# Optimization experiments

Hardware: AMD Instinct MI355X
Metric: run time of the kernel (lower is better)

Reference implementation:

```python
import jax, jax.numpy as jnp
import numpy as np

THRESHOLD = 0.005


def _build_laplacian(x, threshold=THRESHOLD):
    # x: [B, C, F]; cosine-correlation adjacency over channels, built with no grad.
    norm = jnp.sqrt(jnp.sum(x * x, axis=2, keepdims=True))          # [B, C, 1]
    denom = jnp.einsum('bcx,bdx->bcd', norm, norm)                  # [B, C, C]
    num = jnp.einsum('bcf,bdf->bcd', x, x)                          # [B, C, C]
    corr = num / denom
    A = jnp.where(jax.nn.relu(corr) > threshold, 1.0, 0.0)          # binarized adjacency
    deg = jnp.sum(A, axis=2)                                        # [B, C]; >=1 (self-corr==1)
    d_inv_sqrt = 1.0 / jnp.sqrt(deg)
    # D^{-1/2} A D^{-1/2} as elementwise row/col scaling (diag inverse is reciprocal)
    L = A * d_inv_sqrt[:, :, None] * d_inv_sqrt[:, None, :]
    return jax.lax.stop_gradient(L)


def setup_inputs() -> dict:
    key = jax.random.key(0)
    k = jax.random.split(key, 5)
    F = 512
    stdv = 1.0 / np.sqrt(F)
    x = jax.random.normal(k[0], (8, 2048, F), dtype=jnp.float32)
    W1 = jax.random.uniform(k[1], (1, F, F), dtype=jnp.float32, minval=-stdv, maxval=stdv)
    b1 = jax.random.uniform(k[2], (1,), dtype=jnp.float32, minval=-stdv, maxval=stdv)
    W2 = jax.random.uniform(k[3], (1, F, F), dtype=jnp.float32, minval=-stdv, maxval=stdv)
    b2 = jax.random.uniform(k[4], (1,), dtype=jnp.float32, minval=-stdv, maxval=stdv)
    return {"x": x, "W1": W1, "b1": b1, "W2": W2, "b2": b2}


def reference(x, W1, b1, W2, b2):
    L = _build_laplacian(x)                                         # [B, C, C]
    h = x                                                           # [B, C, F]
    for W, b in ((W1, b1), (W2, b2)):
        lx = jnp.einsum('bcd,bdf->bcf', L, h)                       # graph propagation
        h = jax.nn.relu(jnp.einsum('bcf,fg->bcg', lx, W[0]) + b)    # linear + scalar bias + relu
    return h
```

## Files before the change

kernel.cpp:

```cpp
#include <hip/hip_runtime.h>
#include <hip/hip_bf16.h>
#include <cstdint>
#include <cstddef>

#define B_ 8
#define C_ 2048
#define F_ 512
#define TTILES 32
#define NPAIRS 528
#define BAND 0.015f
#define FLAGCAP (1u << 18)

typedef short bf16x8 __attribute__((ext_vector_type(8)));
typedef float f32x4 __attribute__((ext_vector_type(4)));


__device__ __forceinline__ ushort bf16hi(float v) {
  return __builtin_bit_cast(unsigned short, __float2bfloat16(v));
}

__device__ __forceinline__ int swz2048(int flat) {
  return (flat & 7) * 256 + (flat >> 3);
}

__global__ __launch_bounds__(64) void kzero1(uint32_t* __restrict__ flagn) {
  if (threadIdx.x == 0) *flagn = 0u;
}

__global__ __launch_bounds__(256) void ksplit(const float* __restrict__ x,
                                              ushort* __restrict__ xhi,
                                              ushort* __restrict__ xlo) {
  size_t i = ((size_t)blockIdx.x * 256 + threadIdx.x) * 8;
  float4 v0 = *reinterpret_cast<const float4*>(x + i);
  float4 v1 = *reinterpret_cast<const float4*>(x + i + 4);
  float vv[8] = {v0.x, v0.y, v0.z, v0.w, v1.x, v1.y, v1.z, v1.w};
  ushort h[8], lo[8];
#pragma unroll
  for (int j = 0; j < 8; ++j) {
    ushort hh = bf16hi(vv[j]);
    float hf = __bfloat162float(__builtin_bit_cast(__hip_bfloat16, hh));
    h[j] = hh; lo[j] = bf16hi(vv[j] - hf);
  }
  *reinterpret_cast<uint4*>(xhi + i) = *reinterpret_cast<uint4*>(h);
  *reinterpret_cast<uint4*>(xlo + i) = *reinterpret_cast<uint4*>(lo);
}

__global__ __launch_bounds__(256) void kwsplit(const float* __restrict__ W1,
                                               const float* __restrict__ W2,
                                               ushort* __restrict__ wtbuf) {
  const float* W = blockIdx.z ? W2 : W1;
  ushort* whi = wtbuf + (size_t)blockIdx.z * 524288;
  ushort* wlo = whi + 262144;
  int k0 = blockIdx.x * 64, n0 = blockIdx.y * 64, tid = threadIdx.x;
  __shared__ float t[64][65];
#pragma unroll
// ... 15 lines not shown
      float v = t[g * 8 + j][n];
      ushort hh = bf16hi(v);
      float hf = __bfloat162float(__builtin_bit_cast(__hip_bfloat16, hh));
      h8[j] = hh; l8[j] = bf16hi(v - hf);
    }
    size_t ga = (size_t)(n0 + n) * 512 + k0 + g * 8;
    *reinterpret_cast<uint4*>(&whi[ga]) = *reinterpret_cast<uint4*>(h8);
    *reinterpret_cast<uint4*>(&wlo[ga]) = *reinterpret_cast<uint4*>(l8);
  }
}

__global__ __launch_bounds__(256) void knorm(const float* __restrict__ x,
                                             double* __restrict__ nrm) {
  int row = blockIdx.x * 4 + (threadIdx.x >> 6);
  int lane = threadIdx.x & 63;
  const float4* xr = reinterpret_cast<const float4*>(x + (size_t)row * F_);
  float4 v1 = xr[lane];
  float4 v2 = xr[lane + 64];
  double s = (double)v1.x * v1.x + (double)v1.y * v1.y +
             (double)v1.z * v1.z + (double)v1.w * v1.w +
             (double)v2.x * v2.x + (double)v2.y * v2.y +
             (double)v2.z * v2.z + (double)v2.w * v2.w;
#pragma unroll
  for (int off = 32; off > 0; off >>= 1) s += __shfl_down(s, off, 64);
  if (lane == 0) nrm[row] = sqrt(s);
}

__global__ __launch_bounds__(256) void kgram2(const ushort* __restrict__ xhi,
                                              const ushort* __restrict__ xlo,
                                              const double* __restrict__ nrm,
                                              uint32_t* __restrict__ bits,
                                              uint32_t* __restrict__ flagn,
                                              uint32_t* __restrict__ flags) {
  int b = blockIdx.y;
  int tt = (int)blockIdx.x, I = 0;
  while (tt >= TTILES - I) { tt -= TTILES - I; ++I; }
  int J = I + tt;
  bool offdiag = (I != J);
  int c0 = I * 64, d0 = J * 64;
  int tid = threadIdx.x;
  int l = tid & 63, w = tid >> 6;
  int wc = w >> 1, wf = w & 1;
  int lg = l >> 4, li = l & 15;

  __shared__ ushort sm[4 * 64 * 64];
  __shared__ uint32_t lb[64][2];
  __shared__ uint32_t lbT[64][2];

  f32x4 acc[2][2];
#pragma unroll
  for (int m = 0; m < 2; ++m)
#pragma unroll
    for (int n = 0; n < 2; ++n) acc[m][n] = (f32x4){0.f, 0.f, 0.f, 0.f};

  const size_t xbase = (size_t)b * C_ * F_;

  for (int kc = 0; kc < F_ / 64; ++kc) {
    __syncthreads();
#pragma unroll
    for (int s = 0; s < 8; ++s) {
      int is = w + s * 4;
      int tile = is >> 3, sub = is & 7;
      const ushort* src = (tile & 1) ? xlo : xhi;
      int rbase = (tile < 2) ? c0 : d0;
      int row = sub * 8 + (l >> 3);
      int g = l & 7;
      uint4 v = *reinterpret_cast<const uint4*>(
          src + xbase + (size_t)(rbase + row) * F_ + kc * 64 + g * 8);
      int ldsoff = tile * 4096 + row * 64 + ((g ^ (row & 7)) * 8);
      *reinterpret_cast<uint4*>(&sm[ldsoff]) = v;
    }
    __syncthreads();
#pragma unroll
    for (int kk = 0; kk < 2; ++kk) {
      bf16x8 ah[2], al[2], bh[2], bl[2];
#pragma unroll
      for (int m = 0; m < 2; ++m) {
        int row = wc * 32 + m * 16 + li;
        int off = row * 64 + (((kk * 4 + lg) ^ (row & 7)) * 8);
        ah[m] = *reinterpret_cast<const bf16x8*>(&sm[off]);
        al[m] = *reinterpret_cast<const bf16x8*>(&sm[4096 + off]);
      }
#pragma unroll
      for (int n = 0; n < 2; ++n) {
        int row = wf * 32 + n * 16 + li;
        int off = row * 64 + (((kk * 4 + lg) ^ (row & 7)) * 8);
        bh[n] = *reinterpret_cast<const bf16x8*>(&sm[8192 + off]);
        bl[n] = *reinterpret_cast<const bf16x8*>(&sm[12288 + off]);
      }
#pragma unroll
      for (int m = 0; m < 2; ++m)
#pragma unroll
        for (int n = 0; n < 2; ++n) {
          acc[m][n] = __builtin_amdgcn_mfma_f32_16x16x32_bf16(ah[m], bh[n], acc[m][n], 0, 0, 0);
          acc[m][n] = __builtin_amdgcn_mfma_f32_16x16x32_bf16(ah[m], bl[n], acc[m][n], 0, 0, 0);
          acc[m][n] = __builtin_amdgcn_mfma_f32_16x16x32_bf16(al[m], bh[n], acc[m][n], 0, 0, 0);
        }
    }
  }

  double ncv[2][4], ndv[2];
#pragma unroll
  for (int m = 0; m < 2; ++m)
#pragma unroll
    for (int q = 0; q < 4; ++q)
      ncv[m][q] = nrm[b * C_ + c0 + wc * 32 + m * 16 + lg * 4 + q];
#pragma unroll
  for (int n = 0; n < 2; ++n)
    ndv[n] = nrm[b * C_ + d0 + wf * 32 + n * 16 + li];

#pragma unroll
  for (int m = 0; m < 2; ++m) {
#pragma unroll
    for (int q = 0; q < 4; ++q) {
      uint32_t wv = 0;
#pragma unroll
      for (int n = 0; n < 2; ++n) {
        float num = acc[m][n][q];
        float tq = (float)(0.005 * ncv[m][q] * ndv[n]);
        bool bit = num > tq;
        if (fabsf(num - tq) < BAND) {
          uint32_t idx = atomicAdd(flagn, 1u);
          if (idx < FLAGCAP) {
            int cc = c0 + wc * 32 + m * 16 + lg * 4 + q;
            int dd = d0 + wf * 32 + n * 16 + li;
            flags[idx] = ((uint32_t)b << 22) | ((uint32_t)cc << 11) | (uint32_t)dd;
          }
        }
        unsigned long long bal = __ballot(bit);
        uint32_t b16 = (uint32_t)((bal >> (lg * 16)) & 0xFFFFull);
        wv |= b16 << (n * 16);
// ... 43 lines not shown
#pragma unroll
    for (int off = 32; off > 0; off >>= 1) s += __shfl_down(s, off, 64);
    if (l == 0) {
      bool bit = s > 0.005 * nrm[b * C_ + c] * nrm[b * C_ + d];
      uint32_t* wcd = bits + (((size_t)b * C_ + c) << 6) + (d >> 5);
      uint32_t* wdc = bits + (((size_t)b * C_ + d) << 6) + (c >> 5);
      uint32_t mcd = 1u << (d & 31), mdc = 1u << (c & 31);
      if (bit) { atomicOr(wcd, mcd);  atomicOr(wdc, mdc); }
      else     { atomicAnd(wcd, ~mcd); atomicAnd(wdc, ~mdc); }
    }
  }
}

__global__ __launch_bounds__(256) void kdeg(const uint32_t* __restrict__ bits,
                                            float* __restrict__ sinv) {
  int row = blockIdx.x * 256 + threadIdx.x;
  const uint4* p = reinterpret_cast<const uint4*>(bits + ((size_t)row << 6));
  uint32_t s = 0;
#pragma unroll
  for (int i = 0; i < 16; ++i) {
    uint4 v = p[i];
    s += __popc(v.x) + __popc(v.y) + __popc(v.z) + __popc(v.w);
  }
  sinv[row] = 1.0f / sqrtf((float)s);
}

__global__ __launch_bounds__(256) void kgemm_mfma(const ushort* __restrict__ ahi,
                                                  const ushort* __restrict__ alo,
                                                  const ushort* __restrict__ wthi,
                                                  const ushort* __restrict__ wtlo,
                                                  const float* __restrict__ sinv,
                                                  ushort* __restrict__ gthi,
                                                  ushort* __restrict__ gtlo) {
  int flat = (int)blockIdx.y * 256 + (int)blockIdx.x;
  int nid = swz2048(flat);
  int m0 = (nid & 255) * 64, n0 = (nid >> 8) * 64;
  int tid = threadIdx.x;
  int l = tid & 63, w = tid >> 6;
  int wc = w >> 1, wf = w & 1;
  int lg = l >> 4, li = l & 15;

  __shared__ ushort smA[2 * 4096];
  __shared__ ushort smW[2 * 4096];

  f32x4 acc[2][2];
#pragma unroll
  for (int m = 0; m < 2; ++m)
#pragma unroll
    for (int n = 0; n < 2; ++n) acc[m][n] = (f32x4){0.f, 0.f, 0.f, 0.f};

  for (int kc = 0; kc < 8; ++kc) {
    int k0 = kc * 64;
    __syncthreads();
#pragma unroll
    for (int it = 0; it < 2; ++it) {
      int slot = tid + it * 256;
      int row = slot >> 3, grp = slot & 7;
      int loff = row * 64 + ((grp ^ (row & 7)) * 8);
      size_t ga = (size_t)(m0 + row) * 512 + k0 + grp * 8;
      *reinterpret_cast<uint4*>(&smA[loff])        = *reinterpret_cast<const uint4*>(ahi + ga);
      *reinterpret_cast<uint4*>(&smA[4096 + loff]) = *reinterpret_cast<const uint4*>(alo + ga);
      size_t gw = (size_t)(n0 + row) * 512 + k0 + grp * 8;
      *reinterpret_cast<uint4*>(&smW[loff])        = *reinterpret_cast<const uint4*>(wthi + gw);
      *reinterpret_cast<uint4*>(&smW[4096 + loff]) = *reinterpret_cast<const uint4*>(wtlo + gw);
    }
    __syncthreads();
#pragma unroll
    for (int kk = 0; kk < 2; ++kk) {
      bf16x8 ah[2], al[2], wh[2], wl[2];
#pragma unroll
      for (int m = 0; m < 2; ++m) {
        int row = wc * 32 + m * 16 + li;
        int off = row * 64 + (((kk * 4 + lg) ^ (row & 7)) * 8);
        ah[m] = *reinterpret_cast<const bf16x8*>(&smA[off]);
        al[m] = *reinterpret_cast<const bf16x8*>(&smA[4096 + off]);
      }
#pragma unroll
      for (int n = 0; n < 2; ++n) {
        int row = wf * 32 + n * 16 + li;
        int off = row * 64 + (((kk * 4 + lg) ^ (row & 7)) * 8);
        wh[n] = *reinterpret_cast<const bf16x8*>(&smW[off]);
        wl[n] = *reinterpret_cast<const bf16x8*>(&smW[4096 + off]);
      }
#pragma unroll
      for (int m = 0; m < 2; ++m)
#pragma unroll
        for (int n = 0; n < 2; ++n) {
          acc[m][n] = __builtin_amdgcn_mfma_f32_16x16x32_bf16(ah[m], wh[n], acc[m][n], 0, 0, 0);
          acc[m][n] = __builtin_amdgcn_mfma_f32_16x16x32_bf16(ah[m], wl[n], acc[m][n], 0, 0, 0);
          acc[m][n] = __builtin_amdgcn_mfma_f32_16x16x32_bf16(al[m], wh[n], acc[m][n], 0, 0, 0);
          acc[m][n] = __builtin_amdgcn_mfma_f32_16x16x32_bf16(al[m], wl[n], acc[m][n], 0, 0, 0);
        }
    }
  }

  int b = m0 >> 11, cb = m0 & 2047;
#pragma unroll
  for (int m = 0; m < 2; ++m) {
    int rowl = wc * 32 + m * 16 + lg * 4;
    f32x4 sc = *reinterpret_cast<const f32x4*>(&sinv[m0 + rowl]);
#pragma unroll
    for (int n = 0; n < 2; ++n) {
      int f = n0 + wf * 32 + n * 16 + li;
      ushort h4[4], l4[4];
#pragma unroll
      for (int q = 0; q < 4; ++q) {
        float v = sc[q] * acc[m][n][q];
        ushort hh = bf16hi(v);
        float hf = __bfloat162float(__builtin_bit_cast(__hip_bfloat16, hh));
        h4[q] = hh; l4[q] = bf16hi(v - hf);
      }
      size_t ga = ((size_t)b * F_ + f) * C_ + cb + rowl;
      *reinterpret_cast<ushort4*>(&gthi[ga]) = *reinterpret_cast<ushort4*>(h4);
      *reinterpret_cast<ushort4*>(&gtlo[ga]) = *reinterpret_cast<ushort4*>(l4);
    }
  }
}

__global__ __launch_bounds__(256) void kprop_mfma(const ushort* __restrict__ gthi,
                                                  const ushort* __restrict__ gtlo,
                                                  const float* __restrict__ sinv,
                                                  const uint32_t* __restrict__ bits,
                                                  const float* __restrict__ bias,
                                                  ushort* __restrict__ ohi,
                                                  ushort* __restrict__ olo,
                                                  float* __restrict__ of32) {
  int nid = swz2048((int)blockIdx.x);
  int c0 = (nid & 31) * 64, f0 = ((nid >> 5) & 7) * 64, b = nid >> 8;
  int tid = threadIdx.x;
  int l = tid & 63, w = tid >> 6;
  int wc = w >> 1, wf = w & 1;
  int lg = l >> 4, li = l & 15;

  __shared__ ushort smv[2 * 4096];
  __shared__ uint32_t blds[64][68];

  const uint32_t* bp = bits + (((size_t)b * C_ + c0) << 6);
#pragma unroll
  for (int t = 0; t < 4; ++t) {
    int gi = (t * 256 + tid) * 4;
    uint4 q = *reinterpret_cast<const uint4*>(bp + gi);
    int row = gi >> 6, col = gi & 63;
    *reinterpret_cast<uint4*>(&blds[row][col]) = q;
  }

  f32x4 acc[2][2];
#pragma unroll
  for (int m = 0; m < 2; ++m)
#pragma unroll
    for (int n = 0; n < 2; ++n) acc[m][n] = (f32x4){0.f, 0.f, 0.f, 0.f};

  const float* sv = sinv + b * C_;

  for (int d0 = 0; d0 < C_; d0 += 64) {
    __syncthreads();
#pragma unroll
    for (int it = 0; it < 2; ++it) {
      int slot = tid + it * 256;
      int row = slot >> 3, grp = slot & 7;
      int loff = row * 64 + ((grp ^ (row & 7)) * 8);
      size_t ga = ((size_t)b * F_ + f0 + row) * C_ + d0 + grp * 8;
      *reinterpret_cast<uint4*>(&smv[loff])        = *reinterpret_cast<const uint4*>(gthi + ga);
      *reinterpret_cast<uint4*>(&smv[4096 + loff]) = *reinterpret_cast<const uint4*>(gtlo + ga);
    }
    __syncthreads();

    int wbase = d0 >> 5;
#pragma unroll
    for (int kk = 0; kk < 2; ++kk) {
      uint32_t wd0 = blds[wc * 32 + li][wbase + kk];
      uint32_t wd1 = blds[wc * 32 + 16 + li][wbase + kk];
      uint32_t by0 = (wd0 >> (lg * 8)) & 0xFFu;
      uint32_t by1 = (wd1 >> (lg * 8)) & 0xFFu;
      bf16x8 a0, a1;
#pragma unroll
      for (int j = 0; j < 8; ++j) {
        a0[j] = (short)(((by0 >> j) & 1u) ? 0x3F80 : 0);
        a1[j] = (short)(((by1 >> j) & 1u) ? 0x3F80 : 0);
      }
      bf16x8 bh0, bl0, bh1, bl1;
      {
        int row = wf * 32 + li;
        int off = row * 64 + (((kk * 4 + lg) ^ (row & 7)) * 8);
        bh0 = *reinterpret_cast<const bf16x8*>(&smv[off]);
        bl0 = *reinterpret_cast<const bf16x8*>(&smv[4096 + off]);
      }
      {
        int row = wf * 32 + 16 + li;
        int off = row * 64 + (((kk * 4 + lg) ^ (row & 7)) * 8);
        bh1 = *reinterpret_cast<const bf16x8*>(&smv[off]);
        bl1 = *reinterpret_cast<const bf16x8*>(&smv[4096 + off]);
      }
      acc[0][0] = __builtin_amdgcn_mfma_f32_16x16x32_bf16(a0, bh0, acc[0][0], 0, 0, 0);
      acc[0][0] = __builtin_amdgcn_mfma_f32_16x16x32_bf16(a0, bl0, acc[0][0], 0, 0, 0);
      acc[0][1] = __builtin_amdgcn_mfma_f32_16x16x32_bf16(a0, bh1, acc[0][1], 0, 0, 0);
      acc[0][1] = __builtin_amdgcn_mfma_f32_16x16x32_bf16(a0, bl1, acc[0][1], 0, 0, 0);
      acc[1][0] = __builtin_amdgcn_mfma_f32_16x16x32_bf16(a1, bh0, acc[1][0], 0, 0, 0);
      acc[1][0] = __builtin_amdgcn_mfma_f32_16x16x32_bf16(a1, bl0, acc[1][0], 0, 0, 0);
      acc[1][1] = __builtin_amdgcn_mfma_f32_16x16x32_bf16(a1, bh1, acc[1][1], 0, 0, 0);
      acc[1][1] = __builtin_amdgcn_mfma_f32_16x16x32_bf16(a1, bl1, acc[1][1], 0, 0, 0);
    }
  }

  float bb = bias[0];
#pragma unroll
  for (int m = 0; m < 2; ++m) {
    int rowb = c0 + wc * 32 + m * 16 + lg * 4;
    f32x4 sc = *reinterpret_cast<const f32x4*>(&sv[rowb]);
#pragma unroll
    for (int n = 0; n < 2; ++n) {
      int col = f0 + wf * 32 + n * 16 + li;
      if (of32) {
#pragma unroll
        for (int q = 0; q < 4; ++q) {
          float o = fmaxf(sc[q] * acc[m][n][q] + bb, 0.f);
          of32[((size_t)b * C_ + rowb + q) * F_ + col] = o;
        }
      } else {
#pragma unroll
        for (int q = 0; q < 4; ++q) {
          float o = fmaxf(sc[q] * acc[m][n][q] + bb, 0.f);
          ushort hh = bf16hi(o);
          float hf = __bfloat162float(__builtin_bit_cast(__hip_bfloat16, hh));
          size_t ga = ((size_t)b * C_ + rowb + q) * F_ + col;
          ohi[ga] = hh;
          olo[ga] = bf16hi(o - hf);
        }
      }
    }
  }
}

extern "C" void kernel_launch(void* const* d_in, const int* in_sizes, int n_in,
                              void* d_out, int out_size, void* d_ws, size_t ws_size,
                              hipStream_t stream) {
  (void)in_sizes; (void)n_in; (void)out_size; (void)ws_size;
  const float* x  = (const float*)d_in[0];
  const float* W1 = (const float*)d_in[1];
  const float* b1 = (const float*)d_in[2];
  const float* W2 = (const float*)d_in[3];
  const float* b2 = (const float*)d_in[4];
  float* out = (float*)d_out;

  char* ws = (char*)d_ws;
  double*   nrm   = (double*)(ws);
  uint32_t* bits  = (uint32_t*)(ws + 131072);
  float*    sinv  = (float*)(ws + 4325376);
  uint32_t* flagn = (uint32_t*)(ws + 4390912);
  uint32_t* flags = (uint32_t*)(ws + 4391168);
  ushort*   wt    = (ushort*)(ws + 5439744);
  ushort*   xhi   = (ushort*)(ws + 7536896);
  ushort*   xlo   = (ushort*)(ws + 24314112);
  ushort*   gthi  = (ushort*)(ws + 41091328);
  ushort*   gtlo  = (ushort*)(ws + 57868544);
  ushort*   wt1hi = wt, *wt1lo = wt + 262144, *wt2hi = wt + 524288, *wt2lo = wt + 786432;

  kzero1<<<dim3(1), 64, 0, stream>>>(flagn);
  ksplit<<<dim3(B_ * C_ * F_ / 2048), 256, 0, stream>>>(x, xhi, xlo);
  knorm<<<dim3(B_ * C_ / 4), 256, 0, stream>>>(x, nrm);
  kwsplit<<<dim3(8, 8, 2), 256, 0, stream>>>(W1, W2, wt);
  kgram2<<<dim3(NPAIRS, B_), 256, 0, stream>>>(xhi, xlo, nrm, bits, flagn, flags);
  krepair<<<dim3(256), 256, 0, stream>>>(x, nrm, flagn, flags, bits);
  kdeg<<<dim3(B_ * C_ / 256), 256, 0, stream>>>(bits, sinv);

  kgemm_mfma<<<dim3(256, 8), 256, 0, stream>>>(xhi, xlo, wt1hi, wt1lo, sinv, gthi, gtlo);
  kprop_mfma<<<dim3(2048), 256, 0, stream>>>(gthi, gtlo, sinv, bits, b1, xhi, xlo, nullptr);
  kgemm_mfma<<<dim3(256, 8), 256, 0, stream>>>(xhi, xlo, wt2hi, wt2lo, sinv, gthi, gtlo);
  kprop_mfma<<<dim3(2048), 256, 0, stream>>>(gthi, gtlo, sinv, bits, b2, nullptr, nullptr, out);
}
```

Before: 514.8 us.

## Register-prefetch next K chunk in gram, gemm, and prop kernels; retile prop to 128 rows

The Gram, GEMM and propagation kernels now load the next K chunk from global memory into registers while the current chunk is computed from LDS. This replaces the two-syncthreads load-then-compute pattern with explicit barriers and lgkmcnt waits. The block-to-tile mapping is changed so the batch index is innermost, aiming at XCD/L2 locality. The GEMM epilogue transposes through LDS to make global stores coalesced, and the prop kernel uses 128-row tiles with 4 N-subtiles per wave to reuse each loaded G tile more. The cost is more registers and larger LDS use, which may lower occupancy.

```diff
diff --git a/kernel.cpp b/kernel.cpp
--- a/kernel.cpp
+++ b/kernel.cpp
@@ -17,10 +17,6 @@
 
 __device__ __forceinline__ ushort bf16hi(float v) {
   return __builtin_bit_cast(unsigned short, __float2bfloat16(v));
-}
-
-__device__ __forceinline__ int swz2048(int flat) {
-  return (flat & 7) * 256 + (flat >> 3);
 }
 
 __global__ __launch_bounds__(64) void kzero1(uint32_t* __restrict__ flagn) {
@@ -102,8 +98,9 @@
                                               uint32_t* __restrict__ bits,
                                               uint32_t* __restrict__ flagn,
                                               uint32_t* __restrict__ flags) {
-  int b = blockIdx.y;
-  int tt = (int)blockIdx.x, I = 0;
+  int flat = (int)blockIdx.x;
+  int b = flat & 7;
+  int tt = flat >> 3, I = 0;
   while (tt >= TTILES - I) { tt -= TTILES - I; ++I; }
   int J = I + tt;
   bool offdiag = (I != J);
@@ -125,22 +122,37 @@
 
   const size_t xbase = (size_t)b * C_ * F_;
 
-  for (int kc = 0; kc < F_ / 64; ++kc) {
-    __syncthreads();
-#pragma unroll
-    for (int s = 0; s < 8; ++s) {
-      int is = w + s * 4;
-      int tile = is >> 3, sub = is & 7;
-      const ushort* src = (tile & 1) ? xlo : xhi;
-      int rbase = (tile < 2) ? c0 : d0;
-      int row = sub * 8 + (l >> 3);
-      int g = l & 7;
-      uint4 v = *reinterpret_cast<const uint4*>(
-          src + xbase + (size_t)(rbase + row) * F_ + kc * 64 + g * 8);
-      int ldsoff = tile * 4096 + row * 64 + ((g ^ (row & 7)) * 8);
-      *reinterpret_cast<uint4*>(&sm[ldsoff]) = v;
-    }
-    __syncthreads();
+  const ushort* gs[8]; int lo8[8];
+#pragma unroll
+  for (int s = 0; s < 8; ++s) {
+    int is = w + s * 4;
+    int tile = is >> 3, sub = is & 7;
+    const ushort* src = (tile & 1) ? xlo : xhi;
+    int rbase = (tile < 2) ? c0 : d0;
+    int row = sub * 8 + (l >> 3);
+    int g = l & 7;
+    gs[s] = src + xbase + (size_t)(rbase + row) * F_ + g * 8;
+    lo8[s] = tile * 4096 + row * 64 + ((g ^ (row & 7)) * 8);
+  }
+
+  uint4 rX[2][8];
+#pragma unroll
+  for (int s = 0; s < 8; ++s) rX[0][s] = *reinterpret_cast<const uint4*>(gs[s]);
+
+#pragma unroll
+  for (int kc = 0; kc < 8; ++kc) {
+    int cur = kc & 1;
+    __builtin_amdgcn_sched_barrier(0);
+    __builtin_amdgcn_s_barrier();
+#pragma unroll
+    for (int s = 0; s < 8; ++s)
+      *reinterpret_cast<uint4*>(&sm[lo8[s]]) = rX[cur][s];
+#pragma unroll
+    for (int s = 0; s < 8; ++s)
+      rX[cur ^ 1][s] = *reinterpret_cast<const uint4*>(gs[s] + ((kc + 1) & 7) * 64);
+    asm volatile("s_waitcnt lgkmcnt(0)" ::: "memory");
+    __builtin_amdgcn_sched_barrier(0);
+    __builtin_amdgcn_s_barrier();
 #pragma unroll
     for (int kk = 0; kk < 2; ++kk) {
       bf16x8 ah[2], al[2], bh[2], bl[2];
@@ -276,16 +288,29 @@
                                                   const float* __restrict__ sinv,
                                                   ushort* __restrict__ gthi,
                                                   ushort* __restrict__ gtlo) {
-  int flat = (int)blockIdx.y * 256 + (int)blockIdx.x;
-  int nid = swz2048(flat);
-  int m0 = (nid & 255) * 64, n0 = (nid >> 8) * 64;
+  int flat = (int)blockIdx.x;
+  int b = flat & 7, rest = flat >> 3;
+  int mtl = rest & 31, nt = rest >> 5;
+  int m0 = b * C_ + mtl * 64;
+  int n0 = nt * 64;
   int tid = threadIdx.x;
   int l = tid & 63, w = tid >> 6;
   int wc = w >> 1, wf = w & 1;
   int lg = l >> 4, li = l & 15;
 
-  __shared__ ushort smA[2 * 4096];
-  __shared__ ushort smW[2 * 4096];
+  __shared__ ushort smem[16384];
+
+  int ldso[2];
+  const ushort* gA[2][2]; const ushort* gW[2][2];
+#pragma unroll
+  for (int it = 0; it < 2; ++it) {
+    int slot = tid + it * 256, row = slot >> 3, grp = slot & 7;
+    ldso[it] = row * 64 + ((grp ^ (row & 7)) * 8);
+    size_t ga = (size_t)(m0 + row) * 512 + grp * 8;
+    gA[it][0] = ahi + ga; gA[it][1] = alo + ga;
+    size_t gw = (size_t)(n0 + row) * 512 + grp * 8;
+    gW[it][0] = wthi + gw; gW[it][1] = wtlo + gw;
+  }
 
   f32x4 acc[2][2];
 #pragma unroll
@@ -293,22 +318,38 @@
 #pragma unroll
     for (int n = 0; n < 2; ++n) acc[m][n] = (f32x4){0.f, 0.f, 0.f, 0.f};
 
+  uint4 rA[2][2][2];
+#pragma unroll
+  for (int it = 0; it < 2; ++it) {
+    rA[0][it][0] = *reinterpret_cast<const uint4*>(gA[it][0]);
+    rA[0][it][1] = *reinterpret_cast<const uint4*>(gA[it][1]);
+  }
+
+#pragma unroll
   for (int kc = 0; kc < 8; ++kc) {
+    int cur = kc & 1;
     int k0 = kc * 64;
-    __syncthreads();
+    __builtin_amdgcn_sched_barrier(0);
+    __builtin_amdgcn_s_barrier();
 #pragma unroll
     for (int it = 0; it < 2; ++it) {
-      int slot = tid + it * 256;
-      int row = slot >> 3, grp = slot & 7;
-      int loff = row * 64 + ((grp ^ (row & 7)) * 8);
-      size_t ga = (size_t)(m0 + row) * 512 + k0 + grp * 8;
-      *reinterpret_cast<uint4*>(&smA[loff])        = *reinterpret_cast<const uint4*>(ahi + ga);
-      *reinterpret_cast<uint4*>(&smA[4096 + loff]) = *reinterpret_cast<const uint4*>(alo + ga);
-      size_t gw = (size_t)(n0 + row) * 512 + k0 + grp * 8;
-      *reinterpret_cast<uint4*>(&smW[loff])        = *reinterpret_cast<const uint4*>(wthi + gw);
-      *reinterpret_cast<uint4*>(&smW[4096 + loff]) = *reinterpret_cast<const uint4*>(wtlo + gw);
-    }
-    __syncthreads();
+      *reinterpret_cast<uint4*>(&smem[ldso[it]])        = rA[cur][it][0];
+      *reinterpret_cast<uint4*>(&smem[4096 + ldso[it]]) = rA[cur][it][1];
+    }
+#pragma unroll
+    for (int it = 0; it < 2; ++it) {
+      int nk = ((kc + 1) & 7) * 64;
+      rA[cur ^ 1][it][0] = *reinterpret_cast<const uint4*>(gA[it][0] + nk);
+      rA[cur ^ 1][it][1] = *reinterpret_cast<const uint4*>(gA[it][1] + nk);
+    }
+#pragma unroll
+    for (int it = 0; it < 2; ++it) {
+      *reinterpret_cast<uint4*>(&smem[8192 + ldso[it]])  = *reinterpret_cast<const uint4*>(gW[it][0] + k0);
+      *reinterpret_cast<uint4*>(&smem[12288 + ldso[it]]) = *reinterpret_cast<const uint4*>(gW[it][1] + k0);
+    }
+    asm volatile("s_waitcnt lgkmcnt(0)" ::: "memory");
+    __builtin_amdgcn_sched_barrier(0);
+    __builtin_amdgcn_s_barrier();
 #pragma unroll
     for (int kk = 0; kk < 2; ++kk) {
       bf16x8 ah[2], al[2], wh[2], wl[2];
@@ -316,15 +357,15 @@
       for (int m = 0; m < 2; ++m) {
         int row = wc * 32 + m * 16 + li;
         int off = row * 64 + (((kk * 4 + lg) ^ (row & 7)) * 8);
-        ah[m] = *reinterpret_cast<const bf16x8*>(&smA[off]);
-        al[m] = *reinterpret_cast<const bf16x8*>(&smA[4096 + off]);
+        ah[m] = *reinterpret_cast<const bf16x8*>(&smem[off]);
+        al[m] = *reinterpret_cast<const bf16x8*>(&smem[4096 + off]);
       }
 #pragma unroll
       for (int n = 0; n < 2; ++n) {
         int row = wf * 32 + n * 16 + li;
         int off = row * 64 + (((kk * 4 + lg) ^ (row & 7)) * 8);
-        wh[n] = *reinterpret_cast<const bf16x8*>(&smW[off]);
-        wl[n] = *reinterpret_cast<const bf16x8*>(&smW[4096 + off]);
+        wh[n] = *reinterpret_cast<const bf16x8*>(&smem[8192 + off]);
+        wl[n] = *reinterpret_cast<const bf16x8*>(&smem[12288 + off]);
       }
 #pragma unroll
       for (int m = 0; m < 2; ++m)
@@ -338,14 +379,14 @@
     }
   }
 
-  int b = m0 >> 11, cb = m0 & 2047;
+  __syncthreads();
 #pragma unroll
   for (int m = 0; m < 2; ++m) {
-    int rowl = wc * 32 + m * 16 + lg * 4;
-    f32x4 sc = *reinterpret_cast<const f32x4*>(&sinv[m0 + rowl]);
+    int dl = wc * 32 + m * 16 + lg * 4;
+    f32x4 sc = *reinterpret_cast<const f32x4*>(&sinv[m0 + dl]);
 #pragma unroll
     for (int n = 0; n < 2; ++n) {
-      int f = n0 + wf * 32 + n * 16 + li;
+      int fl = wf * 32 + n * 16 + li;
       ushort h4[4], l4[4];
 #pragma unroll
       for (int q = 0; q < 4; ++q) {
@@ -354,12 +395,70 @@
         float hf = __bfloat162float(__builtin_bit_cast(__hip_bfloat16, hh));
         h4[q] = hh; l4[q] = bf16hi(v - hf);
       }
-      size_t ga = ((size_t)b * F_ + f) * C_ + cb + rowl;
-      *reinterpret_cast<ushort4*>(&gthi[ga]) = *reinterpret_cast<ushort4*>(h4);
-      *reinterpret_cast<ushort4*>(&gtlo[ga]) = *reinterpret_cast<ushort4*>(l4);
-    }
-  }
-}
+      *reinterpret_cast<ushort4*>(&smem[fl * 68 + dl])        = *reinterpret_cast<ushort4*>(h4);
+      *reinterpret_cast<ushort4*>(&smem[4352 + fl * 68 + dl]) = *reinterpret_cast<ushort4*>(l4);
+    }
+  }
+  __syncthreads();
+  {
+    int fl = tid >> 2, seg = tid & 3;
+    int cb = mtl * 64;
+    int lo = fl * 68 + seg * 16;
+    size_t ga = ((size_t)b * F_ + n0 + fl) * C_ + cb + seg * 16;
+    uint4 p0 = *reinterpret_cast<const uint4*>(&smem[lo]);
+    uint4 p1 = *reinterpret_cast<const uint4*>(&smem[lo + 8]);
+    *reinterpret_cast<uint4*>(&gthi[ga])     = p0;
+    *reinterpret_cast<uint4*>(&gthi[ga + 8]) = p1;
+    uint4 q0 = *reinterpret_cast<const uint4*>(&smem[4352 + lo]);
+    uint4 q1 = *reinterpret_cast<const uint4*>(&smem[4352 + lo + 8]);
+    *reinterpret_cast<uint4*>(&gtlo[ga])     = q0;
+    *reinterpret_cast<uint4*>(&gtlo[ga + 8]) = q1;
+  }
+}
+
+#define PROP_CHUNK(D, USE, PF, DN)                                            \
+  {                                                                           \
+    __builtin_amdgcn_sched_barrier(0);                                        \
+    __builtin_amdgcn_s_barrier();                                             \
+    _Pragma("unroll")                                                         \
+    for (int it = 0; it < 2; ++it) {                                          \
+      *reinterpret_cast<uint4*>(&smv[ldso[it]])        = USE[it][0];          \
+      *reinterpret_cast<uint4*>(&smv[4096 + ldso[it]]) = USE[it][1];          \
+    }                                                                         \
+    _Pragma("unroll")                                                         \
+    for (int it = 0; it < 2; ++it) {                                          \
+      PF[it][0] = *reinterpret_cast<const uint4*>(gsh[it] + (DN));            \
+      PF[it][1] = *reinterpret_cast<const uint4*>(gsl[it] + (DN));            \
+    }                                                                         \
+    asm volatile("s_waitcnt lgkmcnt(0)" ::: "memory");                        \
+    __builtin_amdgcn_sched_barrier(0);                                        \
+    __builtin_amdgcn_s_barrier();                                             \
+    int wbase = (D) >> 5;                                                     \
+    _Pragma("unroll")                                                         \
+    for (int kk = 0; kk < 2; ++kk) {                                          \
+      uint32_t wd0 = blds[w32 + li][wbase + kk];                              \
+      uint32_t wd1 = blds[w32 + 16 + li][wbase + kk];                         \
+      uint32_t by0 = (wd0 >> (lg * 8)) & 0xFFu;                               \
+      uint32_t by1 = (wd1 >> (lg * 8)) & 0xFFu;                               \
+      bf16x8 a0, a1;                                                          \
+      _Pragma("unroll")                                                       \
+      for (int j = 0; j < 8; ++j) {                                           \
+        a0[j] = (short)(((by0 >> j) & 1u) ? 0x3F80 : 0);                      \
+        a1[j] = (short)(((by1 >> j) & 1u) ? 0x3F80 : 0);                      \
+      }                                                                       \
+      _Pragma("unroll")                                                       \
+      for (int n = 0; n < 4; ++n) {                                           \
+        int row = n * 16 + li;                                                \
+        int off = row * 64 + (((kk * 4 + lg) ^ (row & 7)) * 8);               \
+        bf16x8 bh = *reinterpret_cast<const bf16x8*>(&smv[off]);              \
+        bf16x8 bl = *reinterpret_cast<const bf16x8*>(&smv[4096 + off]);       \
+        acc[0][n] = __builtin_amdgcn_mfma_f32_16x16x32_bf16(a0, bh, acc[0][n], 0, 0, 0); \
+        acc[0][n] = __builtin_amdgcn_mfma_f32_16x16x32_bf16(a0, bl, acc[0][n], 0, 0, 0); \
+        acc[1][n] = __builtin_amdgcn_mfma_f32_16x16x32_bf16(a1, bh, acc[1][n], 0, 0, 0); \
+        acc[1][n] = __builtin_amdgcn_mfma_f32_16x16x32_bf16(a1, bl, acc[1][n], 0, 0, 0); \
+      }                                                                       \
+    }                                                                         \
+  }
 
 __global__ __launch_bounds__(256) void kprop_mfma(const ushort* __restrict__ gthi,
                                                   const ushort* __restrict__ gtlo,
@@ -369,91 +468,64 @@
                                                   ushort* __restrict__ ohi,
                                                   ushort* __restrict__ olo,
                                                   float* __restrict__ of32) {
-  int nid = swz2048((int)blockIdx.x);
-  int c0 = (nid & 31) * 64, f0 = ((nid >> 5) & 7) * 64, b = nid >> 8;
+  int flat = (int)blockIdx.x;
+  int b = flat & 7, rest = flat >> 3;
+  int ct = rest & 15, ft = rest >> 4;
+  int c0 = ct * 128, f0 = ft * 64;
   int tid = threadIdx.x;
   int l = tid & 63, w = tid >> 6;
-  int wc = w >> 1, wf = w & 1;
   int lg = l >> 4, li = l & 15;
-
-  __shared__ ushort smv[2 * 4096];
-  __shared__ uint32_t blds[64][68];
+  int w32 = w * 32;
+
+  __shared__ ushort smv[8192];
+  __shared__ uint32_t blds[128][68];
 
   const uint32_t* bp = bits + (((size_t)b * C_ + c0) << 6);
 #pragma unroll
-  for (int t = 0; t < 4; ++t) {
+  for (int t = 0; t < 8; ++t) {
     int gi = (t * 256 + tid) * 4;
     uint4 q = *reinterpret_cast<const uint4*>(bp + gi);
     int row = gi >> 6, col = gi & 63;
     *reinterpret_cast<uint4*>(&blds[row][col]) = q;
   }
 
-  f32x4 acc[2][2];
+  int ldso[2];
+  const ushort* gsh[2]; const ushort* gsl[2];
+#pragma unroll
+  for (int it = 0; it < 2; ++it) {
+    int s = tid + it * 256, row = s >> 3, grp = s & 7;
+    ldso[it] = row * 64 + ((grp ^ (row & 7)) * 8);
+    size_t ga = ((size_t)b * F_ + f0 + row) * (size_t)C_ + grp * 8;
+    gsh[it] = gthi + ga; gsl[it] = gtlo + ga;
+  }
+
+  f32x4 acc[2][4];
 #pragma unroll
   for (int m = 0; m < 2; ++m)
 #pragma unroll
-    for (int n = 0; n < 2; ++n) acc[m][n] = (f32x4){0.f, 0.f, 0.f, 0.f};
+    for (int n = 0; n < 4; ++n) acc[m][n] = (f32x4){0.f, 0.f, 0.f, 0.f};
+
+  uint4 rA[2][2], rB[2][2];
+#pragma unroll
+  for (int it = 0; it < 2; ++it) {
+    rA[it][0] = *reinterpret_cast<const uint4*>(gsh[it]);
+    rA[it][1] = *reinterpret_cast<const uint4*>(gsl[it]);
+  }
+
+  for (int d0 = 0; d0 < C_; d0 += 128) {
+    PROP_CHUNK(d0,      rA, rB, d0 + 64);
+    PROP_CHUNK(d0 + 64, rB, rA, (d0 + 128) & (C_ - 1));
+  }
 
   const float* sv = sinv + b * C_;
-
-  for (int d0 = 0; d0 < C_; d0 += 64) {
-    __syncthreads();
-#pragma unroll
-    for (int it = 0; it < 2; ++it) {
-      int slot = tid + it * 256;
-      int row = slot >> 3, grp = slot & 7;
-      int loff = row * 64 + ((grp ^ (row & 7)) * 8);
-      size_t ga = ((size_t)b * F_ + f0 + row) * C_ + d0 + grp * 8;
-      *reinterpret_cast<uint4*>(&smv[loff])        = *reinterpret_cast<const uint4*>(gthi + ga);
-      *reinterpret_cast<uint4*>(&smv[4096 + loff]) = *reinterpret_cast<const uint4*>(gtlo + ga);
-    }
-    __syncthreads();
-
-    int wbase = d0 >> 5;
-#pragma unroll
-    for (int kk = 0; kk < 2; ++kk) {
-      uint32_t wd0 = blds[wc * 32 + li][wbase + kk];
-      uint32_t wd1 = blds[wc * 32 + 16 + li][wbase + kk];
-      uint32_t by0 = (wd0 >> (lg * 8)) & 0xFFu;
-      uint32_t by1 = (wd1 >> (lg * 8)) & 0xFFu;
-      bf16x8 a0, a1;
-#pragma unroll
-      for (int j = 0; j < 8; ++j) {
-        a0[j] = (short)(((by0 >> j) & 1u) ? 0x3F80 : 0);
-        a1[j] = (short)(((by1 >> j) & 1u) ? 0x3F80 : 0);
-      }
-      bf16x8 bh0, bl0, bh1, bl1;
-      {
-        int row = wf * 32 + li;
-        int off = row * 64 + (((kk * 4 + lg) ^ (row & 7)) * 8);
-        bh0 = *reinterpret_cast<const bf16x8*>(&smv[off]);
-        bl0 = *reinterpret_cast<const bf16x8*>(&smv[4096 + off]);
-      }
-      {
-        int row = wf * 32 + 16 + li;
-        int off = row * 64 + (((kk * 4 + lg) ^ (row & 7)) * 8);
-        bh1 = *reinterpret_cast<const bf16x8*>(&smv[off]);
-        bl1 = *reinterpret_cast<const bf16x8*>(&smv[4096 + off]);
-      }
-      acc[0][0] = __builtin_amdgcn_mfma_f32_16x16x32_bf16(a0, bh0, acc[0][0], 0, 0, 0);
-      acc[0][0] = __builtin_amdgcn_mfma_f32_16x16x32_bf16(a0, bl0, acc[0][0], 0, 0, 0);
-      acc[0][1] = __builtin_amdgcn_mfma_f32_16x16x32_bf16(a0, bh1, acc[0][1], 0, 0, 0);
-      acc[0][1] = __builtin_amdgcn_mfma_f32_16x16x32_bf16(a0, bl1, acc[0][1], 0, 0, 0);
-      acc[1][0] = __builtin_amdgcn_mfma_f32_16x16x32_bf16(a1, bh0, acc[1][0], 0, 0, 0);
-      acc[1][0] = __builtin_amdgcn_mfma_f32_16x16x32_bf16(a1, bl0, acc[1][0], 0, 0, 0);
-      acc[1][1] = __builtin_amdgcn_mfma_f32_16x16x32_bf16(a1, bh1, acc[1][1], 0, 0, 0);
-      acc[1][1] = __builtin_amdgcn_mfma_f32_16x16x32_bf16(a1, bl1, acc[1][1], 0, 0, 0);
-    }
-  }
-
   float bb = bias[0];
 #pragma unroll
   for (int m = 0; m < 2; ++m) {
-    int rowb = c0 + wc * 32 + m * 16 + lg * 4;
+    int rowb = c0 + w32 + m * 16 + lg * 4;
     f32x4 sc = *reinterpret_cast<const f32x4*>(&sv[rowb]);
 #pragma unroll
-    for (int n = 0; n < 2; ++n) {
-      int col = f0 + wf * 32 + n * 16 + li;
+    for (int n = 0; n < 4; ++n) {
+      int col = f0 + n * 16 + li;
       if (of32) {
 #pragma unroll
         for (int q = 0; q < 4; ++q) {
@@ -503,12 +575,12 @@
   ksplit<<<dim3(B_ * C_ * F_ / 2048), 256, 0, stream>>>(x, xhi, xlo);
   knorm<<<dim3(B_ * C_ / 4), 256, 0, stream>>>(x, nrm);
   kwsplit<<<dim3(8, 8, 2), 256, 0, stream>>>(W1, W2, wt);
-  kgram2<<<dim3(NPAIRS, B_), 256, 0, stream>>>(xhi, xlo, nrm, bits, flagn, flags);
+  kgram2<<<dim3(NPAIRS * B_), 256, 0, stream>>>(xhi, xlo, nrm, bits, flagn, flags);
   krepair<<<dim3(256), 256, 0, stream>>>(x, nrm, flagn, flags, bits);
   kdeg<<<dim3(B_ * C_ / 256), 256, 0, stream>>>(bits, sinv);
 
-  kgemm_mfma<<<dim3(256, 8), 256, 0, stream>>>(xhi, xlo, wt1hi, wt1lo, sinv, gthi, gtlo);
-  kprop_mfma<<<dim3(2048), 256, 0, stream>>>(gthi, gtlo, sinv, bits, b1, xhi, xlo, nullptr);
-  kgemm_mfma<<<dim3(256, 8), 256, 0, stream>>>(xhi, xlo, wt2hi, wt2lo, sinv, gthi, gtlo);
-  kprop_mfma<<<dim3(2048), 256, 0, stream>>>(gthi, gtlo, sinv, bits, b2, nullptr, nullptr, out);
-}
+  kgemm_mfma<<<dim3(2048), 256, 0, stream>>>(xhi, xlo, wt1hi, wt1lo, sinv, gthi, gtlo);
+  kprop_mfma<<<dim3(1024), 256, 0, stream>>>(gthi, gtlo, sinv, bits, b1, xhi, xlo, nullptr);
+  kgemm_mfma<<<dim3(2048), 256, 0, stream>>>(xhi, xlo, wt2hi, wt2lo, sinv, gthi, gtlo);
+  kprop_mfma<<<dim3(1024), 256, 0, stream>>>(gthi, gtlo, sinv, bits, b2, nullptr, nullptr, out);
+}
```

Result: slower. 785.8 us (+52.6%).

## Double-buffer LDS via direct global-to-LDS loads across gram, gemm and propagation kernels

Applied to the files above, without the earlier changes.

Replaces the register-staged global-to-LDS copies in kgram2, kgemm_mfma and kprop_mfma with global_load_lds direct loads into a double-buffered LDS ring, so the next K-chunk is fetched while the current one feeds MFMA. It also remaps block indices so the batch is the fastest-varying dimension, stages the transposed gemm output through LDS for coalesced 16-byte stores, and doubles the propagation tile to 128 rows per block. The cost is more LDS per block, which may lower occupancy, and it relies on the swizzled source addressing matching the layout the readers expect.

```diff
diff --git a/kernel.cpp b/kernel.cpp
--- a/kernel.cpp
+++ b/kernel.cpp
@@ -19,8 +19,10 @@
   return __builtin_bit_cast(unsigned short, __float2bfloat16(v));
 }
 
-__device__ __forceinline__ int swz2048(int flat) {
-  return (flat & 7) * 256 + (flat >> 3);
+__device__ __forceinline__ void gload16(const void* g, void* l) {
+  __builtin_amdgcn_global_load_lds(
+      (const __attribute__((address_space(1))) void*)g,
+      (__attribute__((address_space(3))) void*)l, 16, 0, 0);
 }
 
 __global__ __launch_bounds__(64) void kzero1(uint32_t* __restrict__ flagn) {
@@ -102,8 +104,9 @@
                                               uint32_t* __restrict__ bits,
                                               uint32_t* __restrict__ flagn,
                                               uint32_t* __restrict__ flags) {
-  int b = blockIdx.y;
-  int tt = (int)blockIdx.x, I = 0;
+  int flat = (int)blockIdx.x;
+  int b = flat & 7;
+  int tt = flat >> 3, I = 0;
   while (tt >= TTILES - I) { tt -= TTILES - I; ++I; }
   int J = I + tt;
   bool offdiag = (I != J);
@@ -112,35 +115,39 @@
   int l = tid & 63, w = tid >> 6;
   int wc = w >> 1, wf = w & 1;
   int lg = l >> 4, li = l & 15;
-
-  __shared__ ushort sm[4 * 64 * 64];
+  int rin = l >> 3, grp = l & 7;
+
+  __shared__ ushort sm[2][16384];
   __shared__ uint32_t lb[64][2];
   __shared__ uint32_t lbT[64][2];
 
+  const size_t xbase = (size_t)b * C_ * F_;
+
+  auto stage = [&](int buf, int kc) {
+#pragma unroll
+    for (int i = 0; i < 8; ++i) {
+      int c = w * 8 + i;
+      int t = c >> 3, sub = c & 7;
+      const ushort* src = (t & 1) ? xlo : xhi;
+      int rbase = (t < 2) ? c0 : d0;
+      int row = sub * 8 + rin;
+      gload16(src + xbase + (size_t)(rbase + row) * F_ + kc * 64 + ((grp ^ rin) << 3),
+              &sm[buf][t * 4096 + sub * 512]);
+    }
+  };
+
   f32x4 acc[2][2];
 #pragma unroll
   for (int m = 0; m < 2; ++m)
 #pragma unroll
     for (int n = 0; n < 2; ++n) acc[m][n] = (f32x4){0.f, 0.f, 0.f, 0.f};
 
-  const size_t xbase = (size_t)b * C_ * F_;
-
-  for (int kc = 0; kc < F_ / 64; ++kc) {
-    __syncthreads();
-#pragma unroll
-    for (int s = 0; s < 8; ++s) {
-      int is = w + s * 4;
-      int tile = is >> 3, sub = is & 7;
-      const ushort* src = (tile & 1) ? xlo : xhi;
-      int rbase = (tile < 2) ? c0 : d0;
-      int row = sub * 8 + (l >> 3);
-      int g = l & 7;
-      uint4 v = *reinterpret_cast<const uint4*>(
-          src + xbase + (size_t)(rbase + row) * F_ + kc * 64 + g * 8);
-      int ldsoff = tile * 4096 + row * 64 + ((g ^ (row & 7)) * 8);
-      *reinterpret_cast<uint4*>(&sm[ldsoff]) = v;
-    }
-    __syncthreads();
+  stage(0, 0);
+  __syncthreads();
+  for (int kc = 0; kc < 8; ++kc) {
+    int buf = kc & 1;
+    if (kc < 7) stage(buf ^ 1, kc + 1);
+    const ushort* sb = sm[buf];
 #pragma unroll
     for (int kk = 0; kk < 2; ++kk) {
       bf16x8 ah[2], al[2], bh[2], bl[2];
@@ -148,15 +155,15 @@
       for (int m = 0; m < 2; ++m) {
         int row = wc * 32 + m * 16 + li;
         int off = row * 64 + (((kk * 4 + lg) ^ (row & 7)) * 8);
-        ah[m] = *reinterpret_cast<const bf16x8*>(&sm[off]);
-        al[m] = *reinterpret_cast<const bf16x8*>(&sm[4096 + off]);
+        ah[m] = *reinterpret_cast<const bf16x8*>(&sb[off]);
+        al[m] = *reinterpret_cast<const bf16x8*>(&sb[4096 + off]);
       }
 #pragma unroll
       for (int n = 0; n < 2; ++n) {
         int row = wf * 32 + n * 16 + li;
         int off = row * 64 + (((kk * 4 + lg) ^ (row & 7)) * 8);
-        bh[n] = *reinterpret_cast<const bf16x8*>(&sm[8192 + off]);
-        bl[n] = *reinterpret_cast<const bf16x8*>(&sm[12288 + off]);
+        bh[n] = *reinterpret_cast<const bf16x8*>(&sb[8192 + off]);
+        bl[n] = *reinterpret_cast<const bf16x8*>(&sb[12288 + off]);
       }
 #pragma unroll
       for (int m = 0; m < 2; ++m)
@@ -167,6 +174,7 @@
           acc[m][n] = __builtin_amdgcn_mfma_f32_16x16x32_bf16(al[m], bh[n], acc[m][n], 0, 0, 0);
         }
     }
+    __syncthreads();
   }
 
   double ncv[2][4], ndv[2];
@@ -276,16 +284,34 @@
                                                   const float* __restrict__ sinv,
                                                   ushort* __restrict__ gthi,
                                                   ushort* __restrict__ gtlo) {
-  int flat = (int)blockIdx.y * 256 + (int)blockIdx.x;
-  int nid = swz2048(flat);
-  int m0 = (nid & 255) * 64, n0 = (nid >> 8) * 64;
+  int flat = (int)blockIdx.x;
+  int b = flat & 7, rest = flat >> 3;
+  int mtl = rest & 31, nt = rest >> 5;
+  int m0 = b * C_ + mtl * 64;
+  int n0 = nt * 64;
   int tid = threadIdx.x;
   int l = tid & 63, w = tid >> 6;
   int wc = w >> 1, wf = w & 1;
   int lg = l >> 4, li = l & 15;
-
-  __shared__ ushort smA[2 * 4096];
-  __shared__ ushort smW[2 * 4096];
+  int rin = l >> 3, grp = l & 7;
+
+  __shared__ ushort sm[2][16384];
+
+  auto stage = [&](int buf, int kc) {
+#pragma unroll
+    for (int i = 0; i < 8; ++i) {
+      int c = w * 8 + i;
+      int t = c >> 3, sub = c & 7;
+      int row = sub * 8 + rin;
+      const ushort* src; size_t rb;
+      if (t == 0)      { src = ahi;  rb = (size_t)(m0 + row) * F_; }
+      else if (t == 1) { src = alo;  rb = (size_t)(m0 + row) * F_; }
+      else if (t == 2) { src = wthi; rb = (size_t)(n0 + row) * F_; }
+      else             { src = wtlo; rb = (size_t)(n0 + row) * F_; }
+      gload16(src + rb + kc * 64 + ((grp ^ rin) << 3),
+              &sm[buf][t * 4096 + sub * 512]);
+    }
+  };
 
   f32x4 acc[2][2];
 #pragma unroll
@@ -293,22 +319,12 @@
 #pragma unroll
     for (int n = 0; n < 2; ++n) acc[m][n] = (f32x4){0.f, 0.f, 0.f, 0.f};
 
+  stage(0, 0);
+  __syncthreads();
   for (int kc = 0; kc < 8; ++kc) {
-    int k0 = kc * 64;
-    __syncthreads();
-#pragma unroll
-    for (int it = 0; it < 2; ++it) {
-      int slot = tid + it * 256;
-      int row = slot >> 3, grp = slot & 7;
-      int loff = row * 64 + ((grp ^ (row & 7)) * 8);
-      size_t ga = (size_t)(m0 + row) * 512 + k0 + grp * 8;
-      *reinterpret_cast<uint4*>(&smA[loff])        = *reinterpret_cast<const uint4*>(ahi + ga);
-      *reinterpret_cast<uint4*>(&smA[4096 + loff]) = *reinterpret_cast<const uint4*>(alo + ga);
-      size_t gw = (size_t)(n0 + row) * 512 + k0 + grp * 8;
-      *reinterpret_cast<uint4*>(&smW[loff])        = *reinterpret_cast<const uint4*>(wthi + gw);
-      *reinterpret_cast<uint4*>(&smW[4096 + loff]) = *reinterpret_cast<const uint4*>(wtlo + gw);
-    }
-    __syncthreads();
+    int buf = kc & 1;
+    if (kc < 7) stage(buf ^ 1, kc + 1);
+    const ushort* sb = sm[buf];
 #pragma unroll
     for (int kk = 0; kk < 2; ++kk) {
       bf16x8 ah[2], al[2], wh[2], wl[2];
@@ -316,15 +332,15 @@
       for (int m = 0; m < 2; ++m) {
         int row = wc * 32 + m * 16 + li;
         int off = row * 64 + (((kk * 4 + lg) ^ (row & 7)) * 8);
-        ah[m] = *reinterpret_cast<const bf16x8*>(&smA[off]);
-        al[m] = *reinterpret_cast<const bf16x8*>(&smA[4096 + off]);
+        ah[m] = *reinterpret_cast<const bf16x8*>(&sb[off]);
+        al[m] = *reinterpret_cast<const bf16x8*>(&sb[4096 + off]);
       }
 #pragma unroll
       for (int n = 0; n < 2; ++n) {
         int row = wf * 32 + n * 16 + li;
         int off = row * 64 + (((kk * 4 + lg) ^ (row & 7)) * 8);
-        wh[n] = *reinterpret_cast<const bf16x8*>(&smW[off]);
-        wl[n] = *reinterpret_cast<const bf16x8*>(&smW[4096 + off]);
+        wh[n] = *reinterpret_cast<const bf16x8*>(&sb[8192 + off]);
+        wl[n] = *reinterpret_cast<const bf16x8*>(&sb[12288 + off]);
       }
 #pragma unroll
       for (int m = 0; m < 2; ++m)
@@ -336,16 +352,17 @@
           acc[m][n] = __builtin_amdgcn_mfma_f32_16x16x32_bf16(al[m], wl[n], acc[m][n], 0, 0, 0);
         }
     }
-  }
-
-  int b = m0 >> 11, cb = m0 & 2047;
+    __syncthreads();
+  }
+
+  ushort* tb = &sm[0][0];
 #pragma unroll
   for (int m = 0; m < 2; ++m) {
-    int rowl = wc * 32 + m * 16 + lg * 4;
-    f32x4 sc = *reinterpret_cast<const f32x4*>(&sinv[m0 + rowl]);
+    int dl = wc * 32 + m * 16 + lg * 4;
+    f32x4 sc = *reinterpret_cast<const f32x4*>(&sinv[m0 + dl]);
 #pragma unroll
     for (int n = 0; n < 2; ++n) {
-      int f = n0 + wf * 32 + n * 16 + li;
+      int fl = wf * 32 + n * 16 + li;
       ushort h4[4], l4[4];
 #pragma unroll
       for (int q = 0; q < 4; ++q) {
@@ -354,10 +371,19 @@
         float hf = __bfloat162float(__builtin_bit_cast(__hip_bfloat16, hh));
         h4[q] = hh; l4[q] = bf16hi(v - hf);
       }
-      size_t ga = ((size_t)b * F_ + f) * C_ + cb + rowl;
-      *reinterpret_cast<ushort4*>(&gthi[ga]) = *reinterpret_cast<ushort4*>(h4);
-      *reinterpret_cast<ushort4*>(&gtlo[ga]) = *reinterpret_cast<ushort4*>(l4);
-    }
+      *reinterpret_cast<ushort4*>(&tb[fl * 72 + dl])        = *reinterpret_cast<ushort4*>(h4);
+      *reinterpret_cast<ushort4*>(&tb[4608 + fl * 72 + dl]) = *reinterpret_cast<ushort4*>(l4);
+    }
+  }
+  __syncthreads();
+  {
+    int fl = tid >> 2, seg = tid & 3;
+    int lo = fl * 72 + seg * 16;
+    size_t ga = ((size_t)b * F_ + n0 + fl) * C_ + mtl * 64 + seg * 16;
+    *reinterpret_cast<uint4*>(&gthi[ga])     = *reinterpret_cast<const uint4*>(&tb[lo]);
+    *reinterpret_cast<uint4*>(&gthi[ga + 8]) = *reinterpret_cast<const uint4*>(&tb[lo + 8]);
+    *reinterpret_cast<uint4*>(&gtlo[ga])     = *reinterpret_cast<const uint4*>(&tb[4608 + lo]);
+    *reinterpret_cast<uint4*>(&gtlo[ga + 8]) = *reinterpret_cast<const uint4*>(&tb[4608 + lo + 8]);
   }
 }
 
@@ -369,51 +395,57 @@
                                                   ushort* __restrict__ ohi,
                                                   ushort* __restrict__ olo,
                                                   float* __restrict__ of32) {
-  int nid = swz2048((int)blockIdx.x);
-  int c0 = (nid & 31) * 64, f0 = ((nid >> 5) & 7) * 64, b = nid >> 8;
+  int flat = (int)blockIdx.x;
+  int b = flat & 7, rest = flat >> 3;
+  int ct = rest & 15, ft = rest >> 4;
+  int c0 = ct * 128, f0 = ft * 64;
   int tid = threadIdx.x;
   int l = tid & 63, w = tid >> 6;
-  int wc = w >> 1, wf = w & 1;
   int lg = l >> 4, li = l & 15;
-
-  __shared__ ushort smv[2 * 4096];
-  __shared__ uint32_t blds[64][68];
+  int rin = l >> 3, grp = l & 7;
+  int w32 = w * 32;
+
+  __shared__ ushort smv[2][8192];
+  __shared__ uint32_t blds[128][68];
 
   const uint32_t* bp = bits + (((size_t)b * C_ + c0) << 6);
 #pragma unroll
-  for (int t = 0; t < 4; ++t) {
+  for (int t = 0; t < 8; ++t) {
     int gi = (t * 256 + tid) * 4;
     uint4 q = *reinterpret_cast<const uint4*>(bp + gi);
     int row = gi >> 6, col = gi & 63;
     *reinterpret_cast<uint4*>(&blds[row][col]) = q;
   }
 
-  f32x4 acc[2][2];
+  auto stage = [&](int buf, int dd) {
+#pragma unroll
+    for (int i = 0; i < 4; ++i) {
+      int c = w * 4 + i;
+      int t = c >> 3, sub = c & 7;
+      const ushort* src = t ? gtlo : gthi;
+      int row = f0 + sub * 8 + rin;
+      gload16(src + ((size_t)b * F_ + row) * C_ + dd + ((grp ^ rin) << 3),
+              &smv[buf][t * 4096 + sub * 512]);
+    }
+  };
+
+  f32x4 acc[2][4];
 #pragma unroll
   for (int m = 0; m < 2; ++m)
 #pragma unroll
-    for (int n = 0; n < 2; ++n) acc[m][n] = (f32x4){0.f, 0.f, 0.f, 0.f};
-
-  const float* sv = sinv + b * C_;
-
-  for (int d0 = 0; d0 < C_; d0 += 64) {
-    __syncthreads();
-#pragma unroll
-    for (int it = 0; it < 2; ++it) {
-      int slot = tid + it * 256;
-      int row = slot >> 3, grp = slot & 7;
-      int loff = row * 64 + ((grp ^ (row & 7)) * 8);
-      size_t ga = ((size_t)b * F_ + f0 + row) * C_ + d0 + grp * 8;
-      *reinterpret_cast<uint4*>(&smv[loff])        = *reinterpret_cast<const uint4*>(gthi + ga);
-      *reinterpret_cast<uint4*>(&smv[4096 + loff]) = *reinterpret_cast<const uint4*>(gtlo + ga);
-    }
-    __syncthreads();
-
-    int wbase = d0 >> 5;
+    for (int n = 0; n < 4; ++n) acc[m][n] = (f32x4){0.f, 0.f, 0.f, 0.f};
+
+  stage(0, 0);
+  __syncthreads();
+  for (int ch = 0; ch < 32; ++ch) {
+    int buf = ch & 1;
+    if (ch < 31) stage(buf ^ 1, (ch + 1) * 64);
+    const ushort* sb = smv[buf];
+    int wbase = ch * 2;
 #pragma unroll
     for (int kk = 0; kk < 2; ++kk) {
-      uint32_t wd0 = blds[wc * 32 + li][wbase + kk];
-      uint32_t wd1 = blds[wc * 32 + 16 + li][wbase + kk];
+      uint32_t wd0 = blds[w32 + li][wbase + kk];
+      uint32_t wd1 = blds[w32 + 16 + li][wbase + kk];
       uint32_t by0 = (wd0 >> (lg * 8)) & 0xFFu;
       uint32_t by1 = (wd1 >> (lg * 8)) & 0xFFu;
       bf16x8 a0, a1;
@@ -422,38 +454,30 @@
         a0[j] = (short)(((by0 >> j) & 1u) ? 0x3F80 : 0);
         a1[j] = (short)(((by1 >> j) & 1u) ? 0x3F80 : 0);
       }
-      bf16x8 bh0, bl0, bh1, bl1;
-      {
-        int row = wf * 32 + li;
+#pragma unroll
+      for (int n = 0; n < 4; ++n) {
+        int row = n * 16 + li;
         int off = row * 64 + (((kk * 4 + lg) ^ (row & 7)) * 8);
-        bh0 = *reinterpret_cast<const bf16x8*>(&smv[off]);
-        bl0 = *reinterpret_cast<const bf16x8*>(&smv[4096 + off]);
-      }
-      {
-        int row = wf * 32 + 16 + li;
-        int off = row * 64 + (((kk * 4 + lg) ^ (row & 7)) * 8);
-        bh1 = *reinterpret_cast<const bf16x8*>(&smv[off]);
-        bl1 = *reinterpret_cast<const bf16x8*>(&smv[4096 + off]);
-      }
-      acc[0][0] = __builtin_amdgcn_mfma_f32_16x16x32_bf16(a0, bh0, acc[0][0], 0, 0, 0);
-      acc[0][0] = __builtin_amdgcn_mfma_f32_16x16x32_bf16(a0, bl0, acc[0][0], 0, 0, 0);
-      acc[0][1] = __builtin_amdgcn_mfma_f32_16x16x32_bf16(a0, bh1, acc[0][1], 0, 0, 0);
-      acc[0][1] = __builtin_amdgcn_mfma_f32_16x16x32_bf16(a0, bl1, acc[0][1], 0, 0, 0);
-      acc[1][0] = __builtin_amdgcn_mfma_f32_16x16x32_bf16(a1, bh0, acc[1][0], 0, 0, 0);
-      acc[1][0] = __builtin_amdgcn_mfma_f32_16x16x32_bf16(a1, bl0, acc[1][0], 0, 0, 0);
-      acc[1][1] = __builtin_amdgcn_mfma_f32_16x16x32_bf16(a1, bh1, acc[1][1], 0, 0, 0);
-      acc[1][1] = __builtin_amdgcn_mfma_f32_16x16x32_bf16(a1, bl1, acc[1][1], 0, 0, 0);
-    }
-  }
-
+        bf16x8 bh = *reinterpret_cast<const bf16x8*>(&sb[off]);
+        bf16x8 bl = *reinterpret_cast<const bf16x8*>(&sb[4096 + off]);
+        acc[0][n] = __builtin_amdgcn_mfma_f32_16x16x32_bf16(a0, bh, acc[0][n], 0, 0, 0);
+        acc[0][n] = __builtin_amdgcn_mfma_f32_16x16x32_bf16(a0, bl, acc[0][n], 0, 0, 0);
+        acc[1][n] = __builtin_amdgcn_mfma_f32_16x16x32_bf16(a1, bh, acc[1][n], 0, 0, 0);
+        acc[1][n] = __builtin_amdgcn_mfma_f32_16x16x32_bf16(a1, bl, acc[1][n], 0, 0, 0);
+      }
+    }
+    __syncthreads();
+  }
+
+  const float* sv = sinv + b * C_;
   float bb = bias[0];
 #pragma unroll
   for (int m = 0; m < 2; ++m) {
-    int rowb = c0 + wc * 32 + m * 16 + lg * 4;
+    int rowb = c0 + w32 + m * 16 + lg * 4;
     f32x4 sc = *reinterpret_cast<const f32x4*>(&sv[rowb]);
 #pragma unroll
-    for (int n = 0; n < 2; ++n) {
-      int col = f0 + wf * 32 + n * 16 + li;
+    for (int n = 0; n < 4; ++n) {
+      int col = f0 + n * 16 + li;
       if (of32) {
 #pragma unroll
         for (int q = 0; q < 4; ++q) {
@@ -503,12 +527,12 @@
   ksplit<<<dim3(B_ * C_ * F_ / 2048), 256, 0, stream>>>(x, xhi, xlo);
   knorm<<<dim3(B_ * C_ / 4), 256, 0, stream>>>(x, nrm);
   kwsplit<<<dim3(8, 8, 2), 256, 0, stream>>>(W1, W2, wt);
-  kgram2<<<dim3(NPAIRS, B_), 256, 0, stream>>>(xhi, xlo, nrm, bits, flagn, flags);
+  kgram2<<<dim3(NPAIRS * B_), 256, 0, stream>>>(xhi, xlo, nrm, bits, flagn, flags);
   krepair<<<dim3(256), 256, 0, stream>>>(x, nrm, flagn, flags, bits);
   kdeg<<<dim3(B_ * C_ / 256), 256, 0, stream>>>(bits, sinv);
 
-  kgemm_mfma<<<dim3(256, 8), 256, 0, stream>>>(xhi, xlo, wt1hi, wt1lo, sinv, gthi, gtlo);
-  kprop_mfma<<<dim3(2048), 256, 0, stream>>>(gthi, gtlo, sinv, bits, b1, xhi, xlo, nullptr);
-  kgemm_mfma<<<dim3(256, 8), 256, 0, stream>>>(xhi, xlo, wt2hi, wt2lo, sinv, gthi, gtlo);
-  kprop_mfma<<<dim3(2048), 256, 0, stream>>>(gthi, gtlo, sinv, bits, b2, nullptr, nullptr, out);
-}
+  kgemm_mfma<<<dim3(2048), 256, 0, stream>>>(xhi, xlo, wt1hi, wt1lo, sinv, gthi, gtlo);
+  kprop_mfma<<<dim3(1024), 256, 0, stream>>>(gthi, gtlo, sinv, bits, b1, xhi, xlo, nullptr);
+  kgemm_mfma<<<dim3(2048), 256, 0, stream>>>(xhi, xlo, wt2hi, wt2lo, sinv, gthi, gtlo);
+  kprop_mfma<<<dim3(1024), 256, 0, stream>>>(gthi, gtlo, sinv, bits, b2, nullptr, nullptr, out);
+}
```

After: 487.7 us. 5.3% less time.
